# Kernel tuning notes

Measured on AMD Instinct MI355X. Metric: run time of the kernel, lower is better.

The kernel has to match this reference:

```python
import jax, jax.numpy as jnp
import numpy as np

H = 8        # num_heads
D = 768      # d_model
DH = D // H  # d_head = 96


def setup_inputs() -> dict:
    key = jax.random.key(0)
    ks = jax.random.split(key, 12)
    B, S = 4, 2048
    s_in = 1.0 / np.sqrt(D)
    s_cat = 1.0 / np.sqrt(D)
    return {
        "input_querys": jax.random.normal(ks[0], (B, S, D), jnp.float32),
        "input_key": jax.random.normal(ks[1], (B, S, D), jnp.float32),
        "input_values": jax.random.normal(ks[2], (B, S, D), jnp.float32),
        # per-head projection weights, stacked over the head axis
        "Wq": jax.random.normal(ks[3], (H, D, DH), jnp.float32) * s_in,
        "bq": jax.random.normal(ks[4], (H, DH), jnp.float32) * s_in,
        "Wk": jax.random.normal(ks[5], (H, D, DH), jnp.float32) * s_in,
        "bk": jax.random.normal(ks[6], (H, DH), jnp.float32) * s_in,
        "Wv": jax.random.normal(ks[7], (H, D, DH), jnp.float32) * s_in,
        "bv": jax.random.normal(ks[8], (H, DH), jnp.float32) * s_in,
        # output linear: (H*DH) -> D
        "Wo": jax.random.normal(ks[9], (H * DH, D), jnp.float32) * s_cat,
        "bo": jax.random.normal(ks[10], (D,), jnp.float32) * s_cat,
    }


def reference(input_querys, input_key, input_values, Wq, bq, Wk, bk, Wv, bv, Wo, bo):
    # Per-head linear projections (vectorized over the head axis)
    # q/k/v: [B,S,D] -> [B,H,S,DH]
    Q = jnp.einsum("bsd,hdk->bhsk", input_querys, Wq) + bq[None, :, None, :]
    K = jnp.einsum("bsd,hdk->bhsk", input_key, Wk) + bk[None, :, None, :]
    V = jnp.einsum("bsd,hdk->bhsk", input_values, Wv) + bv[None, :, None, :]

    scale = 1.0 / jnp.sqrt(jnp.asarray(DH, Q.dtype))
    scores = jnp.einsum("bhsk,bhtk->bhst", Q, K) * scale  # [B,H,S,S]
    attn = jax.nn.softmax(scores, axis=-1)
    out = jnp.einsum("bhst,bhtk->bhsk", attn, V)  # [B,H,S,DH]

    # concat heads (head-major order matches torch.cat over ModuleList)
    B, _, S, _ = out.shape
    cat = out.transpose(0, 2, 1, 3).reshape(B, S, H * DH)
    return cat @ Wo + bo
```

## Files before the change

kernel.cpp:

```cpp
#include <hip/hip_runtime.h>


typedef unsigned short u16;
typedef _Float16 h16;
typedef h16 h16x8 __attribute__((ext_vector_type(8)));
typedef __fp16 fp16x2 __attribute__((ext_vector_type(2)));
typedef unsigned short u16x8 __attribute__((ext_vector_type(8)));
typedef unsigned short u16x4 __attribute__((ext_vector_type(4)));
typedef float f32x4 __attribute__((ext_vector_type(4)));

__device__ __forceinline__ u16 f2h(float f) {
  union { h16 h; u16 u; } c; c.h = (h16)f; return c.u;
}

__device__ __forceinline__ void gll16(const void* g, void* l) {
  __builtin_amdgcn_global_load_lds(
      (const __attribute__((address_space(1))) void*)g,
      (__attribute__((address_space(3))) void*)l, 16, 0, 0);
}

__global__ __launch_bounds__(256) void cvt_kernel(
    const float* __restrict__ X, u16* __restrict__ Y)
{
  int i = (blockIdx.x * 256 + threadIdx.x) * 8;
  f32x4 a = *(const f32x4*)(X + i);
  f32x4 b = *(const f32x4*)(X + i + 4);
  u16x8 hv;
  #pragma unroll
  for (int j = 0; j < 4; j++) { hv[j] = f2h(a[j]); hv[4 + j] = f2h(b[j]); }
  *(u16x8*)(Y + i) = hv;
}

__global__ __launch_bounds__(256) void prep_kernel(
    const float* __restrict__ Wq, const float* __restrict__ Wk,
    const float* __restrict__ Wv, const float* __restrict__ Wo,
    u16* __restrict__ WqT, u16* __restrict__ WkT,
    u16* __restrict__ WvT, u16* __restrict__ WoT)
{
  int idx = (blockIdx.x * 256 + threadIdx.x) * 8;
  int region = idx / 589824;
  int i = idx % 589824;
  int n = i / 768;
  int d = i % 768;
  u16x8 v;
  if (region == 3) {
    #pragma unroll
    for (int j = 0; j < 8; j++) v[j] = f2h(Wo[(size_t)(d + j) * 768 + n]);
    *(u16x8*)(&WoT[i]) = v;
  } else {
    int h = n / 96, kk = n % 96;
    const float* W = (region == 0) ? Wq : (region == 1) ? Wk : Wv;
    u16* T = (region == 0) ? WqT : (region == 1) ? WkT : WvT;
    #pragma unroll
    for (int j = 0; j < 8; j++) v[j] = f2h(W[(size_t)h * 73728 + (size_t)(d + j) * 96 + kk]);
    *(u16x8*)(&T[i]) = v;
  }
}

#define GK 768

template<int OUT_MODE>
__global__ __launch_bounds__(256) void gemm16(
    const u16* __restrict__ A, const u16* __restrict__ BT,
    const float* __restrict__ bias, void* __restrict__ Yv)
{
  __shared__ __align__(16) u16 As[128 * 32];
  __shared__ __align__(16) u16 Bs[64 * 32];
  const int tid = threadIdx.x;
  const int wave = tid >> 6;
  const int lane = tid & 63;
  const int quad = lane >> 4;
  const int l16 = lane & 15;
  const int m0 = blockIdx.x * 128;
  const int n0 = blockIdx.y * 64;

  f32x4 acc[2][4];
  #pragma unroll
  for (int i = 0; i < 2; i++)
    #pragma unroll
    for (int j = 0; j < 4; j++) acc[i][j] = (f32x4){0.f, 0.f, 0.f, 0.f};

  const int Lr = lane >> 2, Lc = (lane & 3) * 8;
  const u16* gA0 = A + (size_t)(m0 + wave * 32 + Lr) * GK + Lc;
  const u16* gA1 = gA0 + (size_t)16 * GK;
  const u16* gB  = BT + (size_t)(n0 + wave * 16 + Lr) * GK + Lc;
  u16* lA0 = &As[(wave * 32) * 32];
  u16* lA1 = &As[(wave * 32 + 16) * 32];
  u16* lB  = &Bs[(wave * 16) * 32];

  for (int kt = 0; kt < 24; kt++) {
    gll16(gA0, lA0);
    gll16(gA1, lA1);
    gll16(gB, lB);
    gA0 += 32; gA1 += 32; gB += 32;
    __syncthreads();

    h16x8 af[2], bf[4];
    #pragma unroll
    for (int mf = 0; mf < 2; mf++)
      af[mf] = *(const h16x8*)(&As[(wave * 32 + mf * 16 + l16) * 32 + quad * 8]);
    #pragma unroll
    for (int nf = 0; nf < 4; nf++)
      bf[nf] = *(const h16x8*)(&Bs[(nf * 16 + l16) * 32 + quad * 8]);
    #pragma unroll
    for (int mf = 0; mf < 2; mf++)
      #pragma unroll
      for (int nf = 0; nf < 4; nf++)
        acc[mf][nf] = __builtin_amdgcn_mfma_f32_16x16x32_f16(af[mf], bf[nf], acc[mf][nf], 0, 0, 0);
    __syncthreads();
  }

  #pragma unroll
  for (int nf = 0; nf < 4; nf++) {
    const int n = n0 + nf * 16 + l16;
    const float bv = bias[n];
    #pragma unroll
    for (int mf = 0; mf < 2; mf++) {
      const int m = m0 + wave * 32 + mf * 16 + quad * 4;
      if (OUT_MODE == 2) {
        const int b = m >> 11, s = m & 2047;
        u16x4 pk;
        #pragma unroll
        for (int r = 0; r < 4; r++) pk[r] = f2h(acc[mf][nf][r] + bv);
        *(u16x4*)(&((u16*)Yv)[(size_t)b * 768 * 2048 + (size_t)n * 2048 + s]) = pk;
      } else {
        #pragma unroll
        for (int r = 0; r < 4; r++) {
          const float val = acc[mf][nf][r] + bv;
          if (OUT_MODE == 1) ((float*)Yv)[(size_t)(m + r) * GK + n] = val;
          else               ((u16*)Yv)[(size_t)(m + r) * GK + n] = f2h(val);
        }
      }
    }
  }
}

#define SEQ 2048
#define LQK 104
#define LVT 72
#define LPS 72

__global__ __launch_bounds__(512, 4) void attn_kernel(
    const u16* __restrict__ Q, const u16* __restrict__ K,
    const u16* __restrict__ VT, u16* __restrict__ O)
{
  __shared__ __align__(16) u16 Ks[64 * LQK];
  __shared__ __align__(16) u16 Vt[96 * LVT];
  __shared__ __align__(16) u16 Ps[8][16 * LPS];

  const int tid = threadIdx.x;
  const int wave = tid >> 6;
  const int lane = tid & 63;
  const int quad = lane >> 4;
  const int l16 = lane & 15;

  const int bh = blockIdx.y;
  const int b = bh >> 3, h = bh & 7;
  const int q0 = blockIdx.x * 128;

  const size_t batch_off = (size_t)b * SEQ * 768;
  const u16* Kg = K + batch_off + h * 96;
  const u16* Vg = VT + (size_t)b * 768 * 2048 + (size_t)(h * 96) * 2048;

  h16x8 qf[3];
  {
    const u16* Qrow = Q + batch_off + (size_t)(q0 + wave * 16 + l16) * 768 + h * 96 + quad * 8;
    #pragma unroll
    for (int ks = 0; ks < 3; ks++) qf[ks] = *(const h16x8*)(&Qrow[ks * 32]);
  }

  const int kr0 = tid / 12, kc0 = (tid % 12) * 8;
  const int kr1 = (tid + 512) / 12, kc1 = ((tid + 512) % 12) * 8;
  const int vr0 = tid >> 3, vc0 = (tid & 7) * 8;
  const int vr1 = (tid + 512) >> 3, vc1 = ((tid + 512) & 7) * 8;
  const bool extra = tid < 256;

  f32x4 o[6];
  #pragma unroll
  for (int i = 0; i < 6; i++) o[i] = (f32x4){0.f, 0.f, 0.f, 0.f};
  float m_raw = -1e30f, lrow = 0.f;
  const float sc = 0.14724498f;

  u16* Pw = &Ps[wave][0];

  u16x8 kA, kB, vA, vB;
  kA = *(const u16x8*)(&Kg[(size_t)kr0 * 768 + kc0]);
  vA = *(const u16x8*)(&Vg[(size_t)vr0 * 2048 + vc0]);
  if (extra) {
    kB = *(const u16x8*)(&Kg[(size_t)kr1 * 768 + kc1]);
    vB = *(const u16x8*)(&Vg[(size_t)vr1 * 2048 + vc1]);
  }

  for (int kt = 0; kt < SEQ / 64; kt++) {
    *(u16x8*)(&Ks[kr0 * LQK + kc0]) = kA;
    *(u16x8*)(&Vt[vr0 * LVT + vc0]) = vA;
    if (extra) {
      *(u16x8*)(&Ks[kr1 * LQK + kc1]) = kB;
      *(u16x8*)(&Vt[vr1 * LVT + vc1]) = vB;
    }
    __syncthreads();

    if (kt + 1 < SEQ / 64) {
      const u16* Kn = Kg + (size_t)(kt + 1) * 64 * 768;
      const u16* Vn = Vg + (size_t)(kt + 1) * 64;
      kA = *(const u16x8*)(&Kn[(size_t)kr0 * 768 + kc0]);
      vA = *(const u16x8*)(&Vn[(size_t)vr0 * 2048 + vc0]);
      if (extra) {
        kB = *(const u16x8*)(&Kn[(size_t)kr1 * 768 + kc1]);
        vB = *(const u16x8*)(&Vn[(size_t)vr1 * 2048 + vc1]);
      }
    }

    f32x4 s[4];
    #pragma unroll
    for (int kf = 0; kf < 4; kf++) s[kf] = (f32x4){0.f, 0.f, 0.f, 0.f};
    #pragma unroll
    for (int ks = 0; ks < 3; ks++) {
      #pragma unroll
      for (int kf = 0; kf < 4; kf++) {
        h16x8 a = *(const h16x8*)(&Ks[(kf * 16 + l16) * LQK + ks * 32 + quad * 8]);
        s[kf] = __builtin_amdgcn_mfma_f32_16x16x32_f16(a, qf[ks], s[kf], 0, 0, 0);
      }
    }

    float mx = s[0][0];
    #pragma unroll
    for (int kf = 0; kf < 4; kf++)
      #pragma unroll
      for (int r = 0; r < 4; r++) mx = fmaxf(mx, s[kf][r]);
    mx = fmaxf(mx, __shfl_xor(mx, 16));
    mx = fmaxf(mx, __shfl_xor(mx, 32));
    const float mold = m_raw;
    m_raw = fmaxf(mold, mx);
    const float c0 = sc * m_raw;
    float ps = 0.f;
    #pragma unroll
    for (int kf = 0; kf < 4; kf++)
      #pragma unroll
      for (int r = 0; r < 4; r++) {
        float p = exp2f(fmaf(s[kf][r], sc, -c0));
        s[kf][r] = p;
        ps += p;
      }
    ps += __shfl_xor(ps, 16);
    ps += __shfl_xor(ps, 32);
    if (__any(m_raw > mold)) {
      const float alpha = exp2f(sc * (mold - m_raw));
      lrow *= alpha;
      #pragma unroll
      for (int nfo = 0; nfo < 6; nfo++)
        #pragma unroll
        for (int r = 0; r < 4; r++) o[nfo][r] *= alpha;
    }
    lrow += ps;

    #pragma unroll
    for (int kf = 0; kf < 4; kf++)
      #pragma unroll
      for (int rp = 0; rp < 4; rp += 2) {
        fp16x2 pk = __builtin_amdgcn_cvt_pkrtz(s[kf][rp], s[kf][rp + 1]);
        *(fp16x2*)(&Pw[l16 * LPS + kf * 16 + quad * 4 + rp]) = pk;
      }

    #pragma unroll
    for (int ks = 0; ks < 2; ks++) {
      h16x8 pfr = *(const h16x8*)(&Pw[l16 * LPS + ks * 32 + quad * 8]);
      #pragma unroll
      for (int nfo = 0; nfo < 6; nfo++) {
        h16x8 vfr = *(const h16x8*)(&Vt[(nfo * 16 + l16) * LVT + ks * 32 + quad * 8]);
        o[nfo] = __builtin_amdgcn_mfma_f32_16x16x32_f16(vfr, pfr, o[nfo], 0, 0, 0);
      }
    }
    __syncthreads();
  }

  const float inv = 1.0f / lrow;
  u16* Ob = O + batch_off + (size_t)(q0 + wave * 16 + l16) * 768 + h * 96;
  #pragma unroll
  for (int nfo = 0; nfo < 6; nfo++) {
    fp16x2 lo = __builtin_amdgcn_cvt_pkrtz(o[nfo][0] * inv, o[nfo][1] * inv);
    fp16x2 hi = __builtin_amdgcn_cvt_pkrtz(o[nfo][2] * inv, o[nfo][3] * inv);
    *(fp16x2*)(&Ob[nfo * 16 + quad * 4]) = lo;
    *(fp16x2*)(&Ob[nfo * 16 + quad * 4 + 2]) = hi;
  }
}

extern "C" void kernel_launch(void* const* d_in, const int* in_sizes, int n_in,
                              void* d_out, int out_size, void* d_ws, size_t ws_size,
                              hipStream_t stream) {
  const float* Xq = (const float*)d_in[0];
  const float* Xk = (const float*)d_in[1];
  const float* Xv = (const float*)d_in[2];
  const float* Wq = (const float*)d_in[3];
  const float* bq = (const float*)d_in[4];
  const float* Wk = (const float*)d_in[5];
  const float* bk = (const float*)d_in[6];
  const float* Wv = (const float*)d_in[7];
  const float* bv = (const float*)d_in[8];
  const float* Wo = (const float*)d_in[9];
  const float* bo = (const float*)d_in[10];

  u16* outu = (u16*)d_out;
  u16* outA = outu;
  u16* outB = outu + 6291456;
  u16* WqT = outB;
  u16* WkT = outB + 589824;
  u16* WvT = outB + 1179648;
  u16* WoT = (u16*)d_ws;

  u16* VTb = (u16*)d_in[2];
  u16* K16 = (u16*)d_in[1];
  u16* Q16 = (u16*)d_in[0];
  u16* A16 = (u16*)d_in[0] + 6291456;

  dim3 ggrid(64, 12);
  prep_kernel<<<1152, 256, 0, stream>>>(Wq, Wk, Wv, Wo, WqT, WkT, WvT, WoT);
  cvt_kernel<<<3072, 256, 0, stream>>>(Xv, outA);
  gemm16<2><<<ggrid, 256, 0, stream>>>(outA, WvT, bv, VTb);
  cvt_kernel<<<3072, 256, 0, stream>>>(Xk, outA);
  gemm16<0><<<ggrid, 256, 0, stream>>>(outA, WkT, bk, K16);
  cvt_kernel<<<3072, 256, 0, stream>>>(Xq, outA);
  gemm16<0><<<ggrid, 256, 0, stream>>>(outA, WqT, bq, Q16);
  attn_kernel<<<dim3(16, 32), 512, 0, stream>>>(Q16, K16, VTb, A16);
  gemm16<1><<<ggrid, 256, 0, stream>>>(A16, WoT, bo, (float*)d_out);
}
```

Measured before the change: 315.3 us.

## Fuse fp32-to-fp16 input conversion into a single batched QKV projection GEMM

Drops the three separate conversion kernels and three projection GEMM launches. A single gemm_qkv kernel now loads fp32 activations, converts them to fp16 in registers, and uses blockIdx.z to select Q, K or V, with a register prefetch of the next k-tile. This removes the fp16 intermediate round trip through global memory and several launches, and it fills the GPU with three times as many blocks. Separately, the softmax row-sum cross-lane shuffle is deferred to after the loop, and buffer placement moves Q16 into the workspace.

```diff
diff --git a/kernel.cpp b/kernel.cpp
--- a/kernel.cpp
+++ b/kernel.cpp
@@ -17,18 +17,6 @@
   __builtin_amdgcn_global_load_lds(
       (const __attribute__((address_space(1))) void*)g,
       (__attribute__((address_space(3))) void*)l, 16, 0, 0);
-}
-
-__global__ __launch_bounds__(256) void cvt_kernel(
-    const float* __restrict__ X, u16* __restrict__ Y)
-{
-  int i = (blockIdx.x * 256 + threadIdx.x) * 8;
-  f32x4 a = *(const f32x4*)(X + i);
-  f32x4 b = *(const f32x4*)(X + i + 4);
-  u16x8 hv;
-  #pragma unroll
-  for (int j = 0; j < 4; j++) { hv[j] = f2h(a[j]); hv[4 + j] = f2h(b[j]); }
-  *(u16x8*)(Y + i) = hv;
 }
 
 __global__ __launch_bounds__(256) void prep_kernel(
@@ -59,10 +47,110 @@
 
 #define GK 768
 
-template<int OUT_MODE>
-__global__ __launch_bounds__(256) void gemm16(
+__global__ __launch_bounds__(256) void gemm_qkv(
+    const float* __restrict__ Xq, const float* __restrict__ Xk,
+    const float* __restrict__ Xv, const u16* __restrict__ WT,
+    const float* __restrict__ bq, const float* __restrict__ bk,
+    const float* __restrict__ bv,
+    u16* __restrict__ Q16, u16* __restrict__ K16, u16* __restrict__ VT)
+{
+  const int z = blockIdx.z;
+  const float* A = (z == 0) ? Xq : (z == 1) ? Xk : Xv;
+  const u16* BT = WT + (size_t)z * 589824;
+  const float* bias = (z == 0) ? bq : (z == 1) ? bk : bv;
+
+  __shared__ __align__(16) u16 As[128 * 32];
+  __shared__ __align__(16) u16 Bs[64 * 32];
+  const int tid = threadIdx.x;
+  const int wave = tid >> 6;
+  const int lane = tid & 63;
+  const int quad = lane >> 4;
+  const int l16 = lane & 15;
+  const int m0 = blockIdx.x * 128;
+  const int n0 = blockIdx.y * 64;
+
+  f32x4 acc[2][4];
+  #pragma unroll
+  for (int i = 0; i < 2; i++)
+    #pragma unroll
+    for (int j = 0; j < 4; j++) acc[i][j] = (f32x4){0.f, 0.f, 0.f, 0.f};
+
+  const int ar = tid >> 2;
+  const int ac = (tid & 3) * 8;
+
+  f32x4 pf[4];
+  u16x8 pb;
+  {
+    pf[0] = *(const f32x4*)(&A[(size_t)(m0 + ar) * GK + ac]);
+    pf[1] = *(const f32x4*)(&A[(size_t)(m0 + ar) * GK + ac + 4]);
+    pf[2] = *(const f32x4*)(&A[(size_t)(m0 + 64 + ar) * GK + ac]);
+    pf[3] = *(const f32x4*)(&A[(size_t)(m0 + 64 + ar) * GK + ac + 4]);
+    pb = *(const u16x8*)(&BT[(size_t)(n0 + ar) * GK + ac]);
+  }
+
+  for (int kt = 0; kt < 24; kt++) {
+    u16x8 h0, h1;
+    #pragma unroll
+    for (int j = 0; j < 4; j++) {
+      h0[j] = f2h(pf[0][j]); h0[4 + j] = f2h(pf[1][j]);
+      h1[j] = f2h(pf[2][j]); h1[4 + j] = f2h(pf[3][j]);
+    }
+    *(u16x8*)(&As[ar * 32 + ac]) = h0;
+    *(u16x8*)(&As[(64 + ar) * 32 + ac]) = h1;
+    *(u16x8*)(&Bs[ar * 32 + ac]) = pb;
+    __syncthreads();
+
+    if (kt + 1 < 24) {
+      const int k0 = (kt + 1) * 32;
+      pf[0] = *(const f32x4*)(&A[(size_t)(m0 + ar) * GK + k0 + ac]);
+      pf[1] = *(const f32x4*)(&A[(size_t)(m0 + ar) * GK + k0 + ac + 4]);
+      pf[2] = *(const f32x4*)(&A[(size_t)(m0 + 64 + ar) * GK + k0 + ac]);
+      pf[3] = *(const f32x4*)(&A[(size_t)(m0 + 64 + ar) * GK + k0 + ac + 4]);
+      pb = *(const u16x8*)(&BT[(size_t)(n0 + ar) * GK + k0 + ac]);
+    }
+
+    h16x8 af[2], bf[4];
+    #pragma unroll
+    for (int mf = 0; mf < 2; mf++)
+      af[mf] = *(const h16x8*)(&As[(wave * 32 + mf * 16 + l16) * 32 + quad * 8]);
+    #pragma unroll
+    for (int nf = 0; nf < 4; nf++)
+      bf[nf] = *(const h16x8*)(&Bs[(nf * 16 + l16) * 32 + quad * 8]);
+    #pragma unroll
+    for (int mf = 0; mf < 2; mf++)
+      #pragma unroll
+      for (int nf = 0; nf < 4; nf++)
+        acc[mf][nf] = __builtin_amdgcn_mfma_f32_16x16x32_f16(af[mf], bf[nf], acc[mf][nf], 0, 0, 0);
+
+    if (kt + 1 < 24) __syncthreads();
+  }
+
+  u16* Yr = (z == 0) ? Q16 : K16;
+  #pragma unroll
+  for (int nf = 0; nf < 4; nf++) {
+    const int n = n0 + nf * 16 + l16;
+    const float bv2 = bias[n];
+    #pragma unroll
+    for (int mf = 0; mf < 2; mf++) {
+      const int m = m0 + wave * 32 + mf * 16 + quad * 4;
+      if (z == 2) {
+        const int b = m >> 11, s = m & 2047;
+        u16x4 pk;
+        #pragma unroll
+        for (int r = 0; r < 4; r++) pk[r] = f2h(acc[mf][nf][r] + bv2);
+        *(u16x4*)(&VT[(size_t)b * 768 * 2048 + (size_t)n * 2048 + s]) = pk;
+      } else {
+        #pragma unroll
+        for (int r = 0; r < 4; r++)
+          Yr[(size_t)(m + r) * GK + n] = f2h(acc[mf][nf][r] + bv2);
+      }
+    }
+  }
+}
+
+__global__ __launch_bounds__(256) void gemm_o(
     const u16* __restrict__ A, const u16* __restrict__ BT,
-    const float* __restrict__ bias, void* __restrict__ Yv)
+    const float* __restrict__ bias, float* __restrict__ Y)
 {
   __shared__ __align__(16) u16 As[128 * 32];
   __shared__ __align__(16) u16 Bs[64 * 32];
@@ -117,20 +205,9 @@
     #pragma unroll
     for (int mf = 0; mf < 2; mf++) {
       const int m = m0 + wave * 32 + mf * 16 + quad * 4;
-      if (OUT_MODE == 2) {
-        const int b = m >> 11, s = m & 2047;
-        u16x4 pk;
-        #pragma unroll
-        for (int r = 0; r < 4; r++) pk[r] = f2h(acc[mf][nf][r] + bv);
-        *(u16x4*)(&((u16*)Yv)[(size_t)b * 768 * 2048 + (size_t)n * 2048 + s]) = pk;
-      } else {
-        #pragma unroll
-        for (int r = 0; r < 4; r++) {
-          const float val = acc[mf][nf][r] + bv;
-          if (OUT_MODE == 1) ((float*)Yv)[(size_t)(m + r) * GK + n] = val;
-          else               ((u16*)Yv)[(size_t)(m + r) * GK + n] = f2h(val);
-        }
-      }
+      #pragma unroll
+      for (int r = 0; r < 4; r++)
+        Y[(size_t)(m + r) * GK + n] = acc[mf][nf][r] + bv;
     }
   }
 }
@@ -242,8 +319,6 @@
         s[kf][r] = p;
         ps += p;
       }
-    ps += __shfl_xor(ps, 16);
-    ps += __shfl_xor(ps, 32);
     if (__any(m_raw > mold)) {
       const float alpha = exp2f(sc * (mold - m_raw));
       lrow *= alpha;
@@ -274,6 +349,8 @@
     __syncthreads();
   }
 
+  lrow += __shfl_xor(lrow, 16);
+  lrow += __shfl_xor(lrow, 32);
   const float inv = 1.0f / lrow;
   u16* Ob = O + batch_off + (size_t)(q0 + wave * 16 + l16) * 768 + h * 96;
   #pragma unroll
@@ -300,27 +377,19 @@
   const float* Wo = (const float*)d_in[9];
   const float* bo = (const float*)d_in[10];
 
+  u16* wsu = (u16*)d_ws;
+  u16* WT  = wsu;
+  u16* WoT = wsu + 3 * 589824;
+  u16* Q16 = wsu + 4 * 589824;
+
   u16* outu = (u16*)d_out;
-  u16* outA = outu;
-  u16* outB = outu + 6291456;
-  u16* WqT = outB;
-  u16* WkT = outB + 589824;
-  u16* WvT = outB + 1179648;
-  u16* WoT = (u16*)d_ws;
-
-  u16* VTb = (u16*)d_in[2];
-  u16* K16 = (u16*)d_in[1];
-  u16* Q16 = (u16*)d_in[0];
-  u16* A16 = (u16*)d_in[0] + 6291456;
-
-  dim3 ggrid(64, 12);
-  prep_kernel<<<1152, 256, 0, stream>>>(Wq, Wk, Wv, Wo, WqT, WkT, WvT, WoT);
-  cvt_kernel<<<3072, 256, 0, stream>>>(Xv, outA);
-  gemm16<2><<<ggrid, 256, 0, stream>>>(outA, WvT, bv, VTb);
-  cvt_kernel<<<3072, 256, 0, stream>>>(Xk, outA);
-  gemm16<0><<<ggrid, 256, 0, stream>>>(outA, WkT, bk, K16);
-  cvt_kernel<<<3072, 256, 0, stream>>>(Xq, outA);
-  gemm16<0><<<ggrid, 256, 0, stream>>>(outA, WqT, bq, Q16);
+  u16* VTb = outu;
+  u16* K16 = outu + 6291456;
+
+  u16* A16 = (u16*)d_in[0];
+
+  prep_kernel<<<1152, 256, 0, stream>>>(Wq, Wk, Wv, Wo, WT, WT + 589824, WT + 2 * 589824, WoT);
+  gemm_qkv<<<dim3(64, 12, 3), 256, 0, stream>>>(Xq, Xk, Xv, WT, bq, bk, bv, Q16, K16, VTb);
   attn_kernel<<<dim3(16, 32), 512, 0, stream>>>(Q16, K16, VTb, A16);
-  gemm16<1><<<ggrid, 256, 0, stream>>>(A16, WoT, bo, (float*)d_out);
-}
+  gemm_o<<<dim3(64, 12), 256, 0, stream>>>(A16, WoT, bo, (float*)d_out);
+}
```

After: 312.0 us. No clear change (-1.0%).
